# Kernel optimization log

Measured on AMD Instinct MI355X. Metric: run time of the kernel, lower is better.

## Reference

```python
import jax, jax.numpy as jnp
import numpy as np

NFRAMES, BS, LATENT = 196, 128, 1024
E = 16            # number of object types (experts)
NJOINTS = 128     # max joints -> padded width
NFEATS = 6
INPUT_FEATS = NJOINTS * NFEATS  # 768


def setup_inputs() -> dict:
    key = jax.random.key(0)
    k1, k2, k3, k4 = jax.random.split(key, 4)
    output = jax.random.normal(k1, (NFRAMES, BS, LATENT), dtype=jnp.float32)
    object_types = jax.random.randint(k2, (BS,), 0, E)
    # stacked per-type Linear params, zero-padded to INPUT_FEATS
    W = jax.random.normal(k3, (E, LATENT, INPUT_FEATS), dtype=jnp.float32) * (1.0 / np.sqrt(LATENT))
    b = jax.random.normal(k4, (E, INPUT_FEATS), dtype=jnp.float32) * 0.01
    # valid joints per type in [8, NJOINTS]
    joint_counts = jax.random.randint(jax.random.fold_in(key, 7), (E,), 8, NJOINTS + 1)
    return {"output": output, "object_types": object_types, "W": W, "b": b,
            "joint_counts": joint_counts}


def reference(output, object_types, W, b, joint_counts):
    # per-expert valid output width and column mask [E, INPUT_FEATS]
    feat_counts = joint_counts * NFEATS
    col_mask = (jnp.arange(INPUT_FEATS)[None, :] < feat_counts[:, None]).astype(output.dtype)
    # gather per-sample expert params: Wg [BS, LATENT, F], bg/mg [BS, F]
    Wg = W[object_types]
    bg = b[object_types]
    mg = col_mask[object_types]
    # y[t,b,f] = sum_d output[t,b,d] * Wg[b,d,f] + bg[b,f], zero-padded past valid width
    y = (jnp.einsum('tbd,bdf->tbf', output, Wg) + bg[None]) * mg[None]
    y = y.reshape(NFRAMES, BS, NJOINTS, NFEATS)
    return jnp.transpose(y, (1, 2, 3, 0))  # (bs, njoints, nfeats, nframes)
```

## Files before the change

kernel.cpp:

```cpp
#include <hip/hip_runtime.h>
#include <hip/hip_bf16.h>


#define NFRAMES 196
#define TPAD    224
#define BSZ     128
#define DLAT    1024
#define FIN     768
#define BM      96
#define BK      32
#define KSTEPS  (DLAT / BK)
#define MTILES  (FIN / BM)
#define NTHREADS 256

typedef short bf16x8 __attribute__((ext_vector_type(8)));
typedef short s16x8  __attribute__((ext_vector_type(8)));
typedef short s16x4  __attribute__((ext_vector_type(4)));
typedef float f32x4  __attribute__((ext_vector_type(4)));

__device__ __forceinline__ int swz(int r) { return ((r >> 1) & 3) ^ ((r >> 3) & 3); }

__device__ __forceinline__ short f2bf(float f) {
    __hip_bfloat16 h = __float2bfloat16(f);
    return __builtin_bit_cast(short, h);
}

#define BAR() do { asm volatile("s_waitcnt lgkmcnt(0)" ::: "memory"); \
                   __builtin_amdgcn_s_barrier(); } while (0)

__global__ __launch_bounds__(NTHREADS, 2)
void fused_expert_gemm(const float* __restrict__ X,
                       const int*   __restrict__ otypes,
                       const float* __restrict__ W,
                       const float* __restrict__ Bias,
                       const int*   __restrict__ jc,
                       float*       __restrict__ out)
{
    __shared__ short As[BM * BK];
    __shared__ short Bs[TPAD * BK];

    const int hw      = blockIdx.x;
    const int logical = (hw & 7) * ((MTILES * BSZ) / 8) + (hw >> 3);
    const int b       = logical >> 3;
    const int mt      = logical & 7;
    const int m0      = mt * BM;

    const int tid  = threadIdx.x;
    const int e    = otypes[b];
    const int wave = tid >> 6;
    const int lane = tid & 63;
    const int lr   = lane & 15;
    const int g    = (lane >> 4) & 3;
    const int wr   = wave >> 1;
    const int wc   = wave & 1;

    const int mb   = tid & 31;
    const int kb   = tid >> 5;
    const bool aact = (mb < 24);
    const int ko = tid & 3;
    const int rw = tid >> 2;

    const f32x4* __restrict__ Xv = reinterpret_cast<const f32x4*>(X);
    const f32x4* __restrict__ Wv = reinterpret_cast<const f32x4*>(W);
    const f32x4 fz = {0.f, 0.f, 0.f, 0.f};

    f32x4 wa[4];
    f32x4 xb[4][2];

    int idxA[3], idxB[7];
    #pragma unroll
    for (int f = 0; f < 3; ++f) {
        const int ma = wr * 48 + f * 16 + lr;
        idxA[f] = ma * BK + 8 * (g ^ swz(ma));
    }
    #pragma unroll
    for (int nf = 0; nf < 7; ++nf) {
        const int nr = wc * 112 + nf * 16 + lr;
        idxB[nf] = nr * BK + 8 * (g ^ swz(nr));
    }
    int idxAw[4];
    #pragma unroll
    for (int j = 0; j < 4; ++j) {
        const int r = (mb + j) & 3;
        const int m = mb * 4 + r;
        idxAw[j] = m * BK + 8 * (((kb >> 1) & 3) ^ swz(m)) + (kb & 1) * 4;
    }
    int idxBw[4];
    #pragma unroll
    for (int p = 0; p < 4; ++p) {
        const int n = p * 64 + rw;
        idxBw[p] = n * BK + 8 * (ko ^ swz(n));
    }

    f32x4 acc[3][7];
    #pragma unroll
    for (int f = 0; f < 3; ++f)
        #pragma unroll
        for (int nf = 0; nf < 7; ++nf) acc[f][nf] = fz;

    auto load_stage = [&](int kk) {
        if (aact) {
            #pragma unroll
            for (int i = 0; i < 4; ++i)
                wa[i] = Wv[(e * DLAT + kk + kb * 4 + i) * (FIN / 4) + (m0 >> 2) + mb];
        }
        #pragma unroll
        for (int p = 0; p < 4; ++p) {
            const int n = p * 64 + rw;
            if (n < NFRAMES) {
                const int base = (n * BSZ + b) * (DLAT / 4) + (kk >> 2) + ko * 2;
                xb[p][0] = Xv[base];
                xb[p][1] = Xv[base + 1];
            } else {
                xb[p][0] = fz; xb[p][1] = fz;
            }
        }
    };

    auto write_stage = [&]() {
        if (aact) {
            #pragma unroll
            for (int j = 0; j < 4; ++j) {
                const int r = (mb + j) & 3;
                s16x4 v;
                v[0] = f2bf(wa[0][r]); v[1] = f2bf(wa[1][r]);
                v[2] = f2bf(wa[2][r]); v[3] = f2bf(wa[3][r]);
                *reinterpret_cast<s16x4*>(&As[idxAw[j]]) = v;
            }
        }
        #pragma unroll
        for (int p = 0; p < 4; ++p) {
            if (p * 64 + rw < TPAD) {
                s16x8 v;
                v[0] = f2bf(xb[p][0][0]); v[1] = f2bf(xb[p][0][1]);
                v[2] = f2bf(xb[p][0][2]); v[3] = f2bf(xb[p][0][3]);
                v[4] = f2bf(xb[p][1][0]); v[5] = f2bf(xb[p][1][1]);
                v[6] = f2bf(xb[p][1][2]); v[7] = f2bf(xb[p][1][3]);
                *reinterpret_cast<s16x8*>(&Bs[idxBw[p]]) = v;
            }
        }
    };

    load_stage(0);

    #pragma unroll 1
    for (int ks = 0; ks < KSTEPS; ++ks) {
        BAR();
        write_stage();
        if (ks + 1 < KSTEPS)
            load_stage((ks + 1) * BK);
        BAR();

        bf16x8 af[3];
        #pragma unroll
        for (int f = 0; f < 3; ++f)
            af[f] = *reinterpret_cast<const bf16x8*>(&As[idxA[f]]);
        #pragma unroll
        for (int nf = 0; nf < 7; ++nf) {
            bf16x8 bv = *reinterpret_cast<const bf16x8*>(&Bs[idxB[nf]]);
            #pragma unroll
            for (int f = 0; f < 3; ++f)
                acc[f][nf] = __builtin_amdgcn_mfma_f32_16x16x32_bf16(af[f], bv, acc[f][nf], 0, 0, 0);
        }
    }

    const int    fcb   = jc[e] * 6;
    const float* biasE = Bias + e * FIN;
    float*       outB  = out + (size_t)b * (FIN * NFRAMES);

    #pragma unroll
    for (int f = 0; f < 3; ++f) {
        #pragma unroll
        for (int rr = 0; rr < 4; ++rr) {
            const int fcol  = m0 + wr * 48 + f * 16 + g * 4 + rr;
            const float bv  = biasE[fcol];
            const bool  val = fcol < fcb;
            #pragma unroll
            for (int nf = 0; nf < 7; ++nf) {
                const int t = wc * 112 + nf * 16 + lr;
                if (t < NFRAMES)
                    outB[fcol * NFRAMES + t] = val ? (acc[f][nf][rr] + bv) : 0.f;
            }
        }
    }
}

extern "C" void kernel_launch(void* const* d_in, const int* in_sizes, int n_in,
                              void* d_out, int out_size, void* d_ws, size_t ws_size,
                              hipStream_t stream) {
    const float* X    = (const float*)d_in[0];
    const int*   ot   = (const int*)d_in[1];
    const float* W    = (const float*)d_in[2];
    const float* Bias = (const float*)d_in[3];
    const int*   jc   = (const int*)d_in[4];
    float*       out  = (float*)d_out;

    dim3 grid(MTILES * BSZ);
    dim3 block(NTHREADS);
    hipLaunchKernelGGL(fused_expert_gemm, grid, block, 0, stream,
                       X, ot, W, Bias, jc, out);
}
```

Measured before the change: 105.9 us.

## Skip masked feature tiles, double-buffer LDS, enlarge M tile, trim frame padding

Blocks whose feature tile lies entirely past the expert's valid width now just write zeros and exit instead of running the GEMM. The M tile grows from 96 to 128 and the frame padding shrinks from 224 to 208, with the second column wave issuing six MFMA columns instead of seven. Shared memory is double-buffered so one barrier per K step suffices. The XOR swizzle is replaced by a rotated k-block write pattern. Occupancy may drop because of the larger accumulator set and doubled LDS.

```diff
diff --git a/kernel.cpp b/kernel.cpp
--- a/kernel.cpp
+++ b/kernel.cpp
@@ -3,30 +3,63 @@
 
 
 #define NFRAMES 196
-#define TPAD    224
+#define TPAD    208
 #define BSZ     128
 #define DLAT    1024
 #define FIN     768
-#define BM      96
+#define BM      128
 #define BK      32
 #define KSTEPS  (DLAT / BK)
 #define MTILES  (FIN / BM)
+#define NBLK    (MTILES * BSZ)
 #define NTHREADS 256
 
 typedef short bf16x8 __attribute__((ext_vector_type(8)));
-typedef short s16x8  __attribute__((ext_vector_type(8)));
-typedef short s16x4  __attribute__((ext_vector_type(4)));
 typedef float f32x4  __attribute__((ext_vector_type(4)));
-
-__device__ __forceinline__ int swz(int r) { return ((r >> 1) & 3) ^ ((r >> 3) & 3); }
-
-__device__ __forceinline__ short f2bf(float f) {
-    __hip_bfloat16 h = __float2bfloat16(f);
-    return __builtin_bit_cast(short, h);
+typedef unsigned int u32x2 __attribute__((ext_vector_type(2)));
+typedef unsigned int u32x4 __attribute__((ext_vector_type(4)));
+
+__device__ __forceinline__ unsigned int pkbf(float lo, float hi) {
+    unsigned short a = (unsigned short)__builtin_bit_cast(short, __float2bfloat16(lo));
+    unsigned short b = (unsigned short)__builtin_bit_cast(short, __float2bfloat16(hi));
+    return (unsigned int)a | ((unsigned int)b << 16);
 }
 
 #define BAR() do { asm volatile("s_waitcnt lgkmcnt(0)" ::: "memory"); \
                    __builtin_amdgcn_s_barrier(); } while (0)
+
+template<int NF>
+__device__ __forceinline__ void mfma_all(const short* __restrict__ Bp, const int* idxB,
+                                         const bf16x8 (&af)[4], f32x4 (&acc)[4][7]) {
+    #pragma unroll
+    for (int nf = 0; nf < NF; ++nf) {
+        bf16x8 bv = *reinterpret_cast<const bf16x8*>(&Bp[idxB[nf]]);
+        #pragma unroll
+        for (int f = 0; f < 4; ++f)
+            acc[f][nf] = __builtin_amdgcn_mfma_f32_16x16x32_bf16(af[f], bv, acc[f][nf], 0, 0, 0);
+    }
+}
+
+template<int NF>
+__device__ __forceinline__ void epilogue(const f32x4 (&acc)[4][7], float* __restrict__ outB,
+                                         const float* __restrict__ biasE, int fcb, int m0,
+                                         int wr, int wc, int g, int lr) {
+    #pragma unroll
+    for (int f = 0; f < 4; ++f) {
+        #pragma unroll
+        for (int rr = 0; rr < 4; ++rr) {
+            const int fcol = m0 + wr * 64 + f * 16 + g * 4 + rr;
+            const float bb = biasE[fcol];
+            const bool  val = fcol < fcb;
+            #pragma unroll
+            for (int nf = 0; nf < NF; ++nf) {
+                const int t = wc * 112 + nf * 16 + lr;
+                if (t < NFRAMES)
+                    outB[fcol * NFRAMES + t] = val ? (acc[f][nf][rr] + bb) : 0.f;
+            }
+        }
+    }
+}
 
 __global__ __launch_bounds__(NTHREADS, 2)
 void fused_expert_gemm(const float* __restrict__ X,
@@ -36,27 +69,38 @@
                        const int*   __restrict__ jc,
                        float*       __restrict__ out)
 {
-    __shared__ short As[BM * BK];
-    __shared__ short Bs[TPAD * BK];
+    __shared__ short As[2][BM * BK];
+    __shared__ short Bs[2][TPAD * BK];
 
     const int hw      = blockIdx.x;
-    const int logical = (hw & 7) * ((MTILES * BSZ) / 8) + (hw >> 3);
-    const int b       = logical >> 3;
-    const int mt      = logical & 7;
+    const int logical = (hw & 7) * (NBLK / 8) + (hw >> 3);
+    const int b       = logical / MTILES;
+    const int mt      = logical - b * MTILES;
     const int m0      = mt * BM;
 
-    const int tid  = threadIdx.x;
-    const int e    = otypes[b];
+    const int tid = threadIdx.x;
+    const int e   = otypes[b];
+    const int fcb = jc[e] * 6;
+    float* outB = out + (size_t)b * (FIN * NFRAMES);
+
+    if (m0 >= fcb) {
+        f32x4 zz = {0.f, 0.f, 0.f, 0.f};
+        f32x4* dst = reinterpret_cast<f32x4*>(outB + m0 * NFRAMES);
+        const int total = (BM * NFRAMES) / 4;
+        for (int i = tid; i < total; i += NTHREADS) dst[i] = zz;
+        return;
+    }
+
     const int wave = tid >> 6;
     const int lane = tid & 63;
     const int lr   = lane & 15;
-    const int g    = (lane >> 4) & 3;
+    const int g    = lane >> 4;
     const int wr   = wave >> 1;
     const int wc   = wave & 1;
 
-    const int mb   = tid & 31;
-    const int kb   = tid >> 5;
-    const bool aact = (mb < 24);
+    const int mb  = tid & 31;
+    const int kb  = tid >> 5;
+    const int kbe = (kb + (mb >> 2)) & 7;
     const int ko = tid & 3;
     const int rw = tid >> 2;
 
@@ -67,43 +111,24 @@
     f32x4 wa[4];
     f32x4 xb[4][2];
 
-    int idxA[3], idxB[7];
-    #pragma unroll
-    for (int f = 0; f < 3; ++f) {
-        const int ma = wr * 48 + f * 16 + lr;
-        idxA[f] = ma * BK + 8 * (g ^ swz(ma));
-    }
-    #pragma unroll
-    for (int nf = 0; nf < 7; ++nf) {
-        const int nr = wc * 112 + nf * 16 + lr;
-        idxB[nf] = nr * BK + 8 * (g ^ swz(nr));
-    }
-    int idxAw[4];
-    #pragma unroll
-    for (int j = 0; j < 4; ++j) {
-        const int r = (mb + j) & 3;
-        const int m = mb * 4 + r;
-        idxAw[j] = m * BK + 8 * (((kb >> 1) & 3) ^ swz(m)) + (kb & 1) * 4;
-    }
-    int idxBw[4];
-    #pragma unroll
-    for (int p = 0; p < 4; ++p) {
-        const int n = p * 64 + rw;
-        idxBw[p] = n * BK + 8 * (ko ^ swz(n));
-    }
-
-    f32x4 acc[3][7];
-    #pragma unroll
-    for (int f = 0; f < 3; ++f)
+    int idxA[4], idxB[7];
+    #pragma unroll
+    for (int f = 0; f < 4; ++f)
+        idxA[f] = (wr * 64 + f * 16 + lr) * BK + g * 8;
+    #pragma unroll
+    for (int nf = 0; nf < 7; ++nf)
+        idxB[nf] = (wc * 112 + nf * 16 + lr) * BK + g * 8;
+
+    f32x4 acc[4][7];
+    #pragma unroll
+    for (int f = 0; f < 4; ++f)
         #pragma unroll
         for (int nf = 0; nf < 7; ++nf) acc[f][nf] = fz;
 
     auto load_stage = [&](int kk) {
-        if (aact) {
-            #pragma unroll
-            for (int i = 0; i < 4; ++i)
-                wa[i] = Wv[(e * DLAT + kk + kb * 4 + i) * (FIN / 4) + (m0 >> 2) + mb];
-        }
+        #pragma unroll
+        for (int i = 0; i < 4; ++i)
+            wa[i] = Wv[(e * DLAT + kk + kbe * 4 + i) * (FIN / 4) + (m0 >> 2) + mb];
         #pragma unroll
         for (int p = 0; p < 4; ++p) {
             const int n = p * 64 + rw;
@@ -111,78 +136,52 @@
                 const int base = (n * BSZ + b) * (DLAT / 4) + (kk >> 2) + ko * 2;
                 xb[p][0] = Xv[base];
                 xb[p][1] = Xv[base + 1];
-            } else {
-                xb[p][0] = fz; xb[p][1] = fz;
+            } else { xb[p][0] = fz; xb[p][1] = fz; }
+        }
+    };
+
+    auto write_stage = [&](int buf) {
+        #pragma unroll
+        for (int jj = 0; jj < 4; ++jj) {
+            const int r = (mb + jj) & 3;
+            u32x2 v = { pkbf(wa[0][r], wa[1][r]), pkbf(wa[2][r], wa[3][r]) };
+            *reinterpret_cast<u32x2*>(&As[buf][(mb * 4 + r) * BK + kbe * 4]) = v;
+        }
+        #pragma unroll
+        for (int p = 0; p < 4; ++p) {
+            const int n = p * 64 + rw;
+            if (n < TPAD) {
+                u32x4 v = { pkbf(xb[p][0][0], xb[p][0][1]), pkbf(xb[p][0][2], xb[p][0][3]),
+                            pkbf(xb[p][1][0], xb[p][1][1]), pkbf(xb[p][1][2], xb[p][1][3]) };
+                *reinterpret_cast<u32x4*>(&Bs[buf][n * BK + ko * 8]) = v;
             }
         }
     };
 
-    auto write_stage = [&]() {
-        if (aact) {
-            #pragma unroll
-            for (int j = 0; j < 4; ++j) {
-                const int r = (mb + j) & 3;
-                s16x4 v;
-                v[0] = f2bf(wa[0][r]); v[1] = f2bf(wa[1][r]);
-                v[2] = f2bf(wa[2][r]); v[3] = f2bf(wa[3][r]);
-                *reinterpret_cast<s16x4*>(&As[idxAw[j]]) = v;
-            }
-        }
-        #pragma unroll
-        for (int p = 0; p < 4; ++p) {
-            if (p * 64 + rw < TPAD) {
-                s16x8 v;
-                v[0] = f2bf(xb[p][0][0]); v[1] = f2bf(xb[p][0][1]);
-                v[2] = f2bf(xb[p][0][2]); v[3] = f2bf(xb[p][0][3]);
-                v[4] = f2bf(xb[p][1][0]); v[5] = f2bf(xb[p][1][1]);
-                v[6] = f2bf(xb[p][1][2]); v[7] = f2bf(xb[p][1][3]);
-                *reinterpret_cast<s16x8*>(&Bs[idxBw[p]]) = v;
-            }
-        }
-    };
-
     load_stage(0);
+    write_stage(0);
+    load_stage(BK);
+    BAR();
 
     #pragma unroll 1
-    for (int ks = 0; ks < KSTEPS; ++ks) {
+    for (int j = 0; j < KSTEPS; ++j) {
+        const int cur = j & 1;
+        bf16x8 af[4];
+        #pragma unroll
+        for (int f = 0; f < 4; ++f)
+            af[f] = *reinterpret_cast<const bf16x8*>(&As[cur][idxA[f]]);
+
+        if (wc == 0) mfma_all<7>(Bs[cur], idxB, af, acc);
+        else         mfma_all<6>(Bs[cur], idxB, af, acc);
+
+        if (j + 1 < KSTEPS) write_stage(cur ^ 1);
+        if (j + 2 < KSTEPS) load_stage((j + 2) * BK);
         BAR();
-        write_stage();
-        if (ks + 1 < KSTEPS)
-            load_stage((ks + 1) * BK);
-        BAR();
-
-        bf16x8 af[3];
-        #pragma unroll
-        for (int f = 0; f < 3; ++f)
-            af[f] = *reinterpret_cast<const bf16x8*>(&As[idxA[f]]);
-        #pragma unroll
-        for (int nf = 0; nf < 7; ++nf) {
-            bf16x8 bv = *reinterpret_cast<const bf16x8*>(&Bs[idxB[nf]]);
-            #pragma unroll
-            for (int f = 0; f < 3; ++f)
-                acc[f][nf] = __builtin_amdgcn_mfma_f32_16x16x32_bf16(af[f], bv, acc[f][nf], 0, 0, 0);
-        }
-    }
-
-    const int    fcb   = jc[e] * 6;
+    }
+
     const float* biasE = Bias + e * FIN;
-    float*       outB  = out + (size_t)b * (FIN * NFRAMES);
-
-    #pragma unroll
-    for (int f = 0; f < 3; ++f) {
-        #pragma unroll
-        for (int rr = 0; rr < 4; ++rr) {
-            const int fcol  = m0 + wr * 48 + f * 16 + g * 4 + rr;
-            const float bv  = biasE[fcol];
-            const bool  val = fcol < fcb;
-            #pragma unroll
-            for (int nf = 0; nf < 7; ++nf) {
-                const int t = wc * 112 + nf * 16 + lr;
-                if (t < NFRAMES)
-                    outB[fcol * NFRAMES + t] = val ? (acc[f][nf][rr] + bv) : 0.f;
-            }
-        }
-    }
+    if (wc == 0) epilogue<7>(acc, outB, biasE, fcb, m0, wr, wc, g, lr);
+    else         epilogue<6>(acc, outB, biasE, fcb, m0, wr, wc, g, lr);
 }
 
 extern "C" void kernel_launch(void* const* d_in, const int* in_sizes, int n_in,
@@ -195,7 +194,7 @@
     const int*   jc   = (const int*)d_in[4];
     float*       out  = (float*)d_out;
 
-    dim3 grid(MTILES * BSZ);
+    dim3 grid(NBLK);
     dim3 block(NTHREADS);
     hipLaunchKernelGGL(fused_expert_gemm, grid, block, 0, stream,
                        X, ot, W, Bias, jc, out);
```

After: 104.6 us. About the same (-1.2%).
